# Optimization experiments

Hardware: AMD Instinct MI355X
Metric: run time of the kernel (lower is better)

Reference implementation:

```python
import jax, jax.numpy as jnp
import numpy as np

N_NODES = 50000
N_EDGES = 600000
NFEAT = 256
NHID = 128
NCLASS = 40


def setup_inputs() -> dict:
    key = jax.random.key(0)
    ks = jax.random.split(key, 10)
    x = jax.random.normal(ks[0], (N_NODES, NFEAT), dtype=jnp.float32)
    edge_src = jax.random.randint(ks[1], (N_EDGES,), 0, N_NODES, dtype=jnp.int32)
    edge_dst = jax.random.randint(ks[2], (N_EDGES,), 0, N_NODES, dtype=jnp.int32)
    # normalized adjacency weights (positive, ~1/deg scale)
    edge_weight = jax.random.uniform(ks[3], (N_EDGES,), dtype=jnp.float32) * 0.2
    # GraphConvolution params (Glorot-ish init)
    W1 = jax.random.normal(ks[4], (NFEAT, NHID), dtype=jnp.float32) / np.float32(np.sqrt(NFEAT))
    b1 = jnp.zeros((NHID,), dtype=jnp.float32)
    W2 = jax.random.normal(ks[5], (NHID, NHID), dtype=jnp.float32) / np.float32(np.sqrt(NHID))
    b2 = jnp.zeros((NHID,), dtype=jnp.float32)
    W3 = jax.random.normal(ks[6], (NHID, NCLASS), dtype=jnp.float32) / np.float32(np.sqrt(NHID))
    b3 = jnp.zeros((NCLASS,), dtype=jnp.float32)
    return {"x": x, "edge_weight": edge_weight, "W1": W1, "b1": b1,
            "W2": W2, "b2": b2, "W3": W3, "b3": b3,
            "edge_src": edge_src, "edge_dst": edge_dst}


def _gcn_layer(h, W, b, edge_src, edge_dst, edge_weight):
    # support = h @ W ; out = spmm(adj, support) + b
    support = h @ W                                   # [N, out]
    msgs = support[edge_src] * edge_weight[:, None]   # [E, out]
    agg = jax.ops.segment_sum(msgs, edge_dst, num_segments=N_NODES)
    return agg + b


def reference(x, edge_weight, W1, b1, W2, b2, W3, b3, edge_src, edge_dst):
    # eval mode: F.dropout(training=False) is identity
    h = jax.nn.relu(_gcn_layer(x, W1, b1, edge_src, edge_dst, edge_weight))
    h = jax.nn.relu(_gcn_layer(h, W2, b2, edge_src, edge_dst, edge_weight))
    h = _gcn_layer(h, W3, b3, edge_src, edge_dst, edge_weight)
    return jax.nn.log_softmax(h, axis=1)
```

## Files before the change

kernel.cpp:

```cpp
#include <hip/hip_runtime.h>
#include <math.h>

#define N_NODES 50000
#define N_EDGES 600000
#define NFEAT   256
#define NHID    128
#define NCLASS  40
#define NBUCK 196
#define EPB_A 2048
#define BUCK_CAP 4096
#define BUCK_WIN 5888
#define BINA_BLOCKS ((N_EDGES + EPB_A - 1) / EPB_A)
#define CVTW_BLOCKS 224
#define GEMM_BLOCKS ((N_NODES + 63) / 64)

typedef __attribute__((ext_vector_type(8))) short bf16x8;
typedef __attribute__((ext_vector_type(4))) float f32x4;
typedef __attribute__((ext_vector_type(2))) float f32x2;

__device__ inline ushort f2bf(float f) {
    uint u = __float_as_uint(f);
    uint r = (u + 0x7fffu + ((u >> 16) & 1u)) >> 16;
    return (ushort)r;
}

__global__ __launch_bounds__(256) void binA_cvtw(const int* __restrict__ src,
                                                 const int* __restrict__ dst,
                                                 const float* __restrict__ w,
                                                 int* __restrict__ bucket_cnt,
                                                 int2* __restrict__ staging, int E,
                                                 const float* __restrict__ W1,
                                                 const float* __restrict__ W2,
                                                 const float* __restrict__ W3,
                                                 ushort* __restrict__ BT1,
                                                 ushort* __restrict__ BT2,
                                                 ushort* __restrict__ BT3) {
    int tid = threadIdx.x;
    if ((int)blockIdx.x >= BINA_BLOCKS) {
        int idx = ((int)blockIdx.x - BINA_BLOCKS) * 256 + tid;
        if (idx < 32768) {
            int nr = idx >> 8, k = idx & 255;
            BT1[idx] = f2bf(W1[(size_t)k * 128 + nr]);
        } else if (idx < 49152) {
            int t = idx - 32768;
            int nr = t >> 7, k = t & 127;
            BT2[t] = f2bf(W2[(size_t)k * 128 + nr]);
        } else if (idx < 57344) {
            int t = idx - 49152;
            int nr = t >> 7, k = t & 127;
            BT3[t] = (nr < 40) ? f2bf(W3[(size_t)k * 40 + nr]) : (ushort)0;
        }
        return;
    }
    __shared__ int lh[NBUCK];
    for (int b = tid; b < NBUCK; b += 256) lh[b] = 0;
    __syncthreads();
    int base = blockIdx.x * EPB_A;
    int d[8];
    #pragma unroll
    for (int j = 0; j < 8; ++j) {
        int i = base + j * 256 + tid;
        d[j] = (i < E) ? dst[i] : -1;
        if (d[j] >= 0) atomicAdd(&lh[d[j] >> 8], 1);
    }
    __syncthreads();
    for (int b = tid; b < NBUCK; b += 256) {
        int c = lh[b];
        lh[b] = c ? (b * BUCK_CAP + atomicAdd(&bucket_cnt[b], c)) : 0;
    }
    __syncthreads();
    #pragma unroll
    for (int j = 0; j < 8; ++j) {
        int i = base + j * 256 + tid;
        if (d[j] >= 0) {
            int slot = atomicAdd(&lh[d[j] >> 8], 1);
            uint rec = ((uint)f2bf(w[i]) << 16) | (uint)src[i];
            staging[slot] = make_int2((int)rec, d[j] & 255);
        }
    }
}

template<int NT, bool AF32>
__device__ __forceinline__ void gemm_body(const void* __restrict__ Ain,
                                          const ushort* __restrict__ BT,
                                          int M, int K, int Nout,
                                          ushort* __restrict__ Cout, int row0) {
    __shared__ ushort a_s[64 * 40];
    __shared__ ushort b_s[64 * NT * 40];
    int tid = threadIdx.x;
    int wave = tid >> 6, lane = tid & 63;
    int lr = lane & 15, lk = (lane >> 4) * 8;
    f32x4 acc[4][NT];
    #pragma unroll
    for (int mt = 0; mt < 4; ++mt)
        #pragma unroll
        for (int nt = 0; nt < NT; ++nt) acc[mt][nt] = (f32x4){0.f, 0.f, 0.f, 0.f};

    for (int k0 = 0; k0 < K; k0 += 32) {
        {
            int r = tid >> 2, c8 = (tid & 3) * 8;
            int gr = row0 + r; if (gr >= M) gr = M - 1;
            if (AF32) {
                const float* Af = (const float*)Ain;
                float4 v0 = *(const float4*)(Af + (size_t)gr * K + k0 + c8);
                float4 v1 = *(const float4*)(Af + (size_t)gr * K + k0 + c8 + 4);
                ushort4 o0, o1;
                o0.x = f2bf(v0.x); o0.y = f2bf(v0.y); o0.z = f2bf(v0.z); o0.w = f2bf(v0.w);
                o1.x = f2bf(v1.x); o1.y = f2bf(v1.y); o1.z = f2bf(v1.z); o1.w = f2bf(v1.w);
                *(ushort4*)(a_s + r * 40 + c8) = o0;
                *(ushort4*)(a_s + r * 40 + c8 + 4) = o1;
            } else {
                const ushort* Ab = (const ushort*)Ain;
                float4 v = *(const float4*)(Ab + (size_t)gr * K + k0 + c8);
                *(float4*)(a_s + r * 40 + c8) = v;
            }
        }
        #pragma unroll
        for (int i = 0; i < NT; ++i) {
            int idx = tid * NT + i;
            int r = idx >> 2, c8 = (idx & 3) * 8;
            float4 v = *(const float4*)(BT + (size_t)r * K + k0 + c8);
            *(float4*)(b_s + r * 40 + c8) = v;
        }
        __syncthreads();
        bf16x8 bfr[NT];
        #pragma unroll
        for (int nt = 0; nt < NT; ++nt)
            bfr[nt] = *(const bf16x8*)(b_s + ((wave * NT + nt) * 16 + lr) * 40 + lk);
        #pragma unroll
        for (int mt = 0; mt < 4; ++mt) {
            bf16x8 afr = *(const bf16x8*)(a_s + (mt * 16 + lr) * 40 + lk);
            #pragma unroll
            for (int nt = 0; nt < NT; ++nt)
                acc[mt][nt] = __builtin_amdgcn_mfma_f32_16x16x32_bf16(
                    afr, bfr[nt], acc[mt][nt], 0, 0, 0);
        }
        __syncthreads();
    }
    int col0 = wave * NT * 16;
    #pragma unroll
    for (int mt = 0; mt < 4; ++mt) {
        int gr0 = row0 + mt * 16 + (lane >> 4) * 4;
        #pragma unroll
        for (int nt = 0; nt < NT; ++nt) {
            int gc = col0 + nt * 16 + lr;
            #pragma unroll
            for (int i = 0; i < 4; ++i) {
                int gr = gr0 + i;
                if (gr < M && gc < Nout)
                    Cout[(size_t)gr * Nout + gc] = f2bf(acc[mt][nt][i]);
            }
        }
    }
}

__global__ __launch_bounds__(256) void scan_gemm1(const int* __restrict__ bucket_cnt,
                                                  const int2* __restrict__ staging,
                                                  int2* __restrict__ rsp2,
                                                  uint* __restrict__ edges,
                                                  const float* __restrict__ x,
                                                  const ushort* __restrict__ BT1,
                                                  ushort* __restrict__ supA) {
    if ((int)blockIdx.x >= NBUCK) {
        gemm_body<2, true>(x, BT1, N_NODES, 256, 128, supA,
                           ((int)blockIdx.x - NBUCK) * 64);
        return;
    }
    __shared__ int hist[256];
    __shared__ int buf[256];
    __shared__ int lcur[256];
    int tid = threadIdx.x;
    hist[tid] = 0;
    __syncthreads();
    int b = blockIdx.x;
    int c = bucket_cnt[b];
    const int2* st = staging + (size_t)b * BUCK_CAP;
    for (int p = tid; p < c; p += 256) atomicAdd(&hist[st[p].y], 1);
    __syncthreads();
    int v = (hist[tid] + 7) & ~7;
    buf[tid] = v;
    __syncthreads();
    #pragma unroll
    for (int off = 1; off < 256; off <<= 1) {
        int t = (tid >= off) ? buf[tid - off] : 0;
        __syncthreads();
        buf[tid] += t;
        __syncthreads();
    }
    int bb = b * BUCK_WIN;
    int ex = buf[tid] - v + bb;
    int i = b * 256 + tid;
    if (i < N_NODES) rsp2[i] = make_int2(ex, ex + v);
    lcur[tid] = ex;
    __syncthreads();
    int e0 = bb + buf[255];
    for (int p = bb + tid; p < e0; p += 256) edges[p] = 0;
    __syncthreads();
    for (int p = tid; p < c; p += 256) {
        int2 r = st[p];
        int slot = atomicAdd(&lcur[r.y], 1);
        edges[slot] = (uint)r.x;
    }
}

template<int NT>
__global__ __launch_bounds__(256) void fused_spmm_gemm(const uint* __restrict__ sup,
                                                       const int2* __restrict__ rsp2,
                                                       const uint* __restrict__ edges,
                                                       const float* __restrict__ bias,
                                                       const ushort* __restrict__ BT,
                                                       int Nout,
                                                       ushort* __restrict__ Cout) {
    __shared__ ushort a4_s[4][64 * 40];
    int tid = threadIdx.x;
    int wave = tid >> 6, lane = tid & 63;
    int row0 = blockIdx.x * 64;
    float bx = bias[2 * lane], by = bias[2 * lane + 1];
    int ks = lane >> 4;
    int kk = 2 * (lane & 15);
    for (int i = 0; i < 16; ++i) {
        int node = row0 + wave * 16 + i;
        int nd = (node < N_NODES) ? node : (N_NODES - 1);
        int2 ke = rsp2[nd];
        int k = ke.x, e = ke.y;
        f32x2 acc2 = (f32x2){0.f, 0.f};
        if (k < e) {
            const uint4* q4 = (const uint4*)(edges + k);
            uint4 qa = q4[0], qb = q4[1];
            for (; k < e; k += 8) {
                int kn = k + 8;
                int kc = (kn < e) ? kn : k;
                const uint4* n4 = (const uint4*)(edges + kc);
                uint4 na = n4[0], nb = n4[1];
                uint q[8] = {qa.x, qa.y, qa.z, qa.w, qb.x, qb.y, qb.z, qb.w};
                uint p[8];
                #pragma unroll
                for (int j = 0; j < 8; ++j)
                    p[j] = sup[(size_t)(q[j] & 0xffffu) * 64 + lane];
                #pragma unroll
                for (int j = 0; j < 8; ++j) {
                    float w = __uint_as_float(q[j] & 0xffff0000u);
                    f32x2 v;
                    v.x = __uint_as_float(p[j] << 16);
                    v.y = __uint_as_float(p[j] & 0xffff0000u);
                    acc2 += v * (f32x2){w, w};
                }
                qa = na; qb = nb;
            }
        }
        uint pk = ((uint)f2bf(fmaxf(acc2.y + by, 0.f)) << 16)
                |  (uint)f2bf(fmaxf(acc2.x + bx, 0.f));
        *(uint*)(&a4_s[ks][(wave * 16 + i) * 40 + kk]) = pk;
    }
    __syncthreads();
    int lr = lane & 15, lk = (lane >> 4) * 8;
    f32x4 acc[4][NT];
    #pragma unroll
    for (int mt = 0; mt < 4; ++mt)
        #pragma unroll
        for (int nt = 0; nt < NT; ++nt) acc[mt][nt] = (f32x4){0.f, 0.f, 0.f, 0.f};
    #pragma unroll
    for (int ksi = 0; ksi < 4; ++ksi) {
        int k0 = ksi * 32;
        bf16x8 bfr[NT];
        #pragma unroll
        for (int nt = 0; nt < NT; ++nt)
            bfr[nt] = *(const bf16x8*)(BT +
                (size_t)((wave * NT + nt) * 16 + lr) * 128 + k0 + lk);
        #pragma unroll
        for (int mt = 0; mt < 4; ++mt) {
            bf16x8 afr = *(const bf16x8*)(&a4_s[ksi][(mt * 16 + lr) * 40 + lk]);
            #pragma unroll
            for (int nt = 0; nt < NT; ++nt)
                acc[mt][nt] = __builtin_amdgcn_mfma_f32_16x16x32_bf16(
                    afr, bfr[nt], acc[mt][nt], 0, 0, 0);
        }
    }
    int col0 = wave * NT * 16;
    #pragma unroll
    for (int mt = 0; mt < 4; ++mt) {
        int gr0 = row0 + mt * 16 + (lane >> 4) * 4;
        #pragma unroll
        for (int nt = 0; nt < NT; ++nt) {
            int gc = col0 + nt * 16 + lr;
            #pragma unroll
            for (int i = 0; i < 4; ++i) {
                int gr = gr0 + i;
                if (gr < N_NODES && gc < Nout)
                    Cout[(size_t)gr * Nout + gc] = f2bf(acc[mt][nt][i]);
            }
        }
    }
}

__global__ __launch_bounds__(256) void spmm40_lsm(const ushort* __restrict__ sup,
                                                  const int2* __restrict__ rsp2,
                                                  const uint* __restrict__ edges,
                                                  const float* __restrict__ bias,
                                                  float* __restrict__ out, int n) {
    int wid = blockIdx.x * 4 + (threadIdx.x >> 6);
    int lane = threadIdx.x & 63;
    if (wid >= n) return;
    int2 ke = rsp2[wid];
    int k = ke.x, e = ke.y;
    float acc = 0.f;
    int lf = (lane < 40) ? lane : 39;
    if (k < e) {
        const uint4* q4 = (const uint4*)(edges + k);
        uint4 qa = q4[0], qb = q4[1];
        for (; k < e; k += 8) {
            int kn = k + 8;
            int kc = (kn < e) ? kn : k;
            const uint4* n4 = (const uint4*)(edges + kc);
            uint4 na = n4[0], nb4 = n4[1];
            uint q[8] = {qa.x, qa.y, qa.z, qa.w, qb.x, qb.y, qb.z, qb.w};
            float p[8];
            #pragma unroll
            for (int j = 0; j < 8; ++j) {
                uint us = sup[(size_t)(q[j] & 0xffffu) * 40 + lf];
                p[j] = __uint_as_float(us << 16);
            }
            #pragma unroll
            for (int j = 0; j < 8; ++j)
                acc += p[j] * __uint_as_float(q[j] & 0xffff0000u);
            qa = na; qb = nb4;
        }
    }
    float v = (lane < 40) ? acc + bias[lane] : -INFINITY;
    float m = v;
    #pragma unroll
    for (int off = 32; off; off >>= 1) m = fmaxf(m, __shfl_xor(m, off, 64));
    float ex = (lane < 40) ? expf(v - m) : 0.f;
    float s = ex;
    #pragma unroll
    for (int off = 32; off; off >>= 1) s += __shfl_xor(s, off, 64);
    float ls = logf(s);
    if (lane < 40) out[(size_t)wid * 40 + lane] = v - m - ls;
}

extern "C" void kernel_launch(void* const* d_in, const int* in_sizes, int n_in,
                              void* d_out, int out_size, void* d_ws, size_t ws_size,
                              hipStream_t stream) {
    const float* x   = (const float*)d_in[0];
    const float* ew  = (const float*)d_in[1];
    const float* W1  = (const float*)d_in[2];
    const float* b1  = (const float*)d_in[3];
    const float* W2  = (const float*)d_in[4];
    const float* b2  = (const float*)d_in[5];
    const float* W3  = (const float*)d_in[6];
    const float* b3  = (const float*)d_in[7];
    const int* esrc  = (const int*)d_in[8];
    const int* edst  = (const int*)d_in[9];
    float* out = (float*)d_out;

    char* ws = (char*)d_ws;
    size_t off = 0;
    auto alloc = [&](size_t bytes) {
        size_t cur = off;
        off += (bytes + 255) & ~(size_t)255;
        return cur;
    };
    int* bucket_cnt = (int*)(ws + alloc(256 * sizeof(int)));
    int2* rsp2   = (int2*)(ws + alloc((size_t)N_NODES * sizeof(int2)));
    uint* edges  = (uint*)(ws + alloc((size_t)NBUCK * BUCK_WIN * sizeof(uint)));
    int2* staging = (int2*)(ws + alloc((size_t)NBUCK * BUCK_CAP * sizeof(int2)));
    ushort* BT1  = (ushort*)(ws + alloc(128 * 256 * 2));
    ushort* BT2  = (ushort*)(ws + alloc(128 * 128 * 2));
    ushort* BT3  = (ushort*)(ws + alloc(64 * 128 * 2));
    char* Sreg   = ws + alloc((size_t)N_NODES * 128 * 2);
    char* Hreg   = ws + alloc((size_t)N_NODES * 128 * 2);

    ushort* supA = (ushort*)Sreg;
    ushort* supB = (ushort*)Hreg;
    ushort* sup3 = (ushort*)Sreg;

    hipMemsetAsync(bucket_cnt, 0, 256 * sizeof(int), stream);
    binA_cvtw<<<BINA_BLOCKS + CVTW_BLOCKS, 256, 0, stream>>>(
        esrc, edst, ew, bucket_cnt, staging, N_EDGES, W1, W2, W3, BT1, BT2, BT3);
    scan_gemm1<<<NBUCK + GEMM_BLOCKS, 256, 0, stream>>>(
        bucket_cnt, staging, rsp2, edges, x, BT1, supA);
    fused_spmm_gemm<2><<<GEMM_BLOCKS, 256, 0, stream>>>(
        (const uint*)supA, rsp2, edges, b1, BT2, 128, supB);
    fused_spmm_gemm<1><<<GEMM_BLOCKS, 256, 0, stream>>>(
        (const uint*)supB, rsp2, edges, b2, BT3, 40, sup3);
    spmm40_lsm<<<(N_NODES + 3) / 4, 256, 0, stream>>>(sup3, rsp2, edges, b3,
                                                      out, N_NODES);
}
```

Measured before the change: 231.2 us.

## Stream each wave's 16-row edge range as one software-pipelined gather loop

The aggregation phase now treats the 16 destination rows of a wave as one contiguous edge range. It loads 16-edge records double-buffered, prefetching the next record and gathering one chunk while accumulating the previous, and flushes each row's result at its segment boundary. This removes the per-row loop startup and pipeline drain, keeping more gathers in flight across short rows. In exchange it needs more registers (two 16-entry buffers), adds a clamp on the gather index for reads past the range, and over-allocates workspace so prefetches beyond the end stay in bounds.

```diff
diff --git a/kernel.cpp b/kernel.cpp
--- a/kernel.cpp
+++ b/kernel.cpp
@@ -203,56 +203,102 @@
     }
 }
 
+
+#define LDREC(Ra, Rb, Rc, Rd, POS) do { \
+    const uint4* _p = (const uint4*)(edges + (POS)); \
+    Ra = _p[0]; Rb = _p[1]; Rc = _p[2]; Rd = _p[3]; \
+} while (0)
+
+#define GATHER(P, W, Ra, Rb, Rc, Rd) do { \
+    uint _r[16] = {Ra.x, Ra.y, Ra.z, Ra.w, Rb.x, Rb.y, Rb.z, Rb.w, \
+                   Rc.x, Rc.y, Rc.z, Rc.w, Rd.x, Rd.y, Rd.z, Rd.w}; \
+    _Pragma("unroll") \
+    for (int _j = 0; _j < 16; ++_j) { \
+        uint _idx = _r[_j] & 0xffffu; \
+        if (_idx >= N_NODES) _idx = N_NODES - 1;   \
+        P[_j] = sup[(size_t)_idx * 64 + lane]; \
+        W[_j] = __uint_as_float(_r[_j] & 0xffff0000u); \
+    } \
+} while (0)
+
+#define FLUSH1() do { \
+    uint _pk = ((uint)f2bf(fmaxf(acc2.y + by, 0.f)) << 16) \
+             |  (uint)f2bf(fmaxf(acc2.x + bx, 0.f)); \
+    *(uint*)(&a4_s[ks][(wave * 16 + cur) * 40 + kk]) = _pk; \
+    acc2 = (f32x2){0.f, 0.f}; \
+    ++cur; \
+    e_cur = (cur < 16) ? e_s[wave][cur + 1] : 0x7fffffff; \
+} while (0)
+
+#define FMA_CHUNK(QB, P, W) do { \
+    _Pragma("unroll") \
+    for (int _g = 0; _g < 2; ++_g) { \
+        int _qg = (QB) + _g * 8; \
+        while (cur < 16 && _qg >= e_cur) FLUSH1(); \
+        if (_qg < QE) { \
+            _Pragma("unroll") \
+            for (int _j = 0; _j < 8; ++_j) { \
+                uint _pv = P[_g * 8 + _j]; \
+                f32x2 _v; \
+                _v.x = __uint_as_float(_pv << 16); \
+                _v.y = __uint_as_float(_pv & 0xffff0000u); \
+                float _w = W[_g * 8 + _j]; \
+                acc2 += _v * (f32x2){_w, _w}; \
+            } \
+        } \
+    } \
+} while (0)
+
 template<int NT>
-__global__ __launch_bounds__(256) void fused_spmm_gemm(const uint* __restrict__ sup,
-                                                       const int2* __restrict__ rsp2,
-                                                       const uint* __restrict__ edges,
-                                                       const float* __restrict__ bias,
-                                                       const ushort* __restrict__ BT,
-                                                       int Nout,
-                                                       ushort* __restrict__ Cout) {
+__device__ __forceinline__ void fused_body(const uint* __restrict__ sup,
+                                           const int2* __restrict__ rsp2,
+                                           const uint* __restrict__ edges,
+                                           const float* __restrict__ bias,
+                                           const ushort* __restrict__ BT,
+                                           int Nout,
+                                           ushort* __restrict__ Cout) {
     __shared__ ushort a4_s[4][64 * 40];
+    __shared__ int e_s[4][17];
     int tid = threadIdx.x;
     int wave = tid >> 6, lane = tid & 63;
     int row0 = blockIdx.x * 64;
+    int nfirst = row0 + wave * 16;
     float bx = bias[2 * lane], by = bias[2 * lane + 1];
     int ks = lane >> 4;
     int kk = 2 * (lane & 15);
-    for (int i = 0; i < 16; ++i) {
-        int node = row0 + wave * 16 + i;
-        int nd = (node < N_NODES) ? node : (N_NODES - 1);
-        int2 ke = rsp2[nd];
-        int k = ke.x, e = ke.y;
-        f32x2 acc2 = (f32x2){0.f, 0.f};
-        if (k < e) {
-            const uint4* q4 = (const uint4*)(edges + k);
-            uint4 qa = q4[0], qb = q4[1];
-            for (; k < e; k += 8) {
-                int kn = k + 8;
-                int kc = (kn < e) ? kn : k;
-                const uint4* n4 = (const uint4*)(edges + kc);
-                uint4 na = n4[0], nb = n4[1];
-                uint q[8] = {qa.x, qa.y, qa.z, qa.w, qb.x, qb.y, qb.z, qb.w};
-                uint p[8];
-                #pragma unroll
-                for (int j = 0; j < 8; ++j)
-                    p[j] = sup[(size_t)(q[j] & 0xffffu) * 64 + lane];
-                #pragma unroll
-                for (int j = 0; j < 8; ++j) {
-                    float w = __uint_as_float(q[j] & 0xffff0000u);
-                    f32x2 v;
-                    v.x = __uint_as_float(p[j] << 16);
-                    v.y = __uint_as_float(p[j] & 0xffff0000u);
-                    acc2 += v * (f32x2){w, w};
-                }
-                qa = na; qb = nb;
-            }
-        }
-        uint pk = ((uint)f2bf(fmaxf(acc2.y + by, 0.f)) << 16)
-                |  (uint)f2bf(fmaxf(acc2.x + bx, 0.f));
-        *(uint*)(&a4_s[ks][(wave * 16 + i) * 40 + kk]) = pk;
-    }
-    __syncthreads();
+
+    if (lane < 16) {
+        int nd = nfirst + lane; if (nd >= N_NODES) nd = N_NODES - 1;
+        int2 t = rsp2[nd];
+        e_s[wave][lane + 1] = t.y;
+        if (lane == 0) e_s[wave][0] = t.x;
+    }
+    __syncthreads();
+    int Q = e_s[wave][0], QE = e_s[wave][16];
+    int cur = 0, e_cur = e_s[wave][1];
+    f32x2 acc2 = (f32x2){0.f, 0.f};
+
+    uint4 rA0, rA1, rA2, rA3, rB0, rB1, rB2, rB3;
+    uint pa[16], pb[16];
+    float wa[16], wb[16];
+    int q = Q;
+    LDREC(rA0, rA1, rA2, rA3, q);
+    GATHER(pa, wa, rA0, rA1, rA2, rA3);
+    LDREC(rB0, rB1, rB2, rB3, q + 16);
+    while (q < QE) {
+        GATHER(pb, wb, rB0, rB1, rB2, rB3);
+        LDREC(rA0, rA1, rA2, rA3, q + 32);
+        FMA_CHUNK(q, pa, wa);
+        q += 16;
+        if (q >= QE) break;
+        GATHER(pa, wa, rA0, rA1, rA2, rA3);
+        LDREC(rB0, rB1, rB2, rB3, q + 32);
+        FMA_CHUNK(q, pb, wb);
+        q += 16;
+    }
+    while (cur < 16) FLUSH1();
+    __syncthreads();
+
     int lr = lane & 15, lk = (lane >> 4) * 8;
     f32x4 acc[4][NT];
     #pragma unroll
@@ -291,6 +337,24 @@
             }
         }
     }
+}
+
+__global__ __launch_bounds__(256) void fused_ag2(const uint* __restrict__ sup,
+                                                 const int2* __restrict__ rsp2,
+                                                 const uint* __restrict__ edges,
+                                                 const float* __restrict__ bias,
+                                                 const ushort* __restrict__ BT,
+                                                 ushort* __restrict__ Cout) {
+    fused_body<2>(sup, rsp2, edges, bias, BT, 128, Cout);
+}
+
+__global__ __launch_bounds__(256) void fused_ag3(const uint* __restrict__ sup,
+                                                 const int2* __restrict__ rsp2,
+                                                 const uint* __restrict__ edges,
+                                                 const float* __restrict__ bias,
+                                                 const ushort* __restrict__ BT,
+                                                 ushort* __restrict__ Cout) {
+    fused_body<1>(sup, rsp2, edges, bias, BT, 40, Cout);
 }
 
 __global__ __launch_bounds__(256) void spmm40_lsm(const ushort* __restrict__ sup,
@@ -369,6 +433,7 @@
     ushort* BT3  = (ushort*)(ws + alloc(64 * 128 * 2));
     char* Sreg   = ws + alloc((size_t)N_NODES * 128 * 2);
     char* Hreg   = ws + alloc((size_t)N_NODES * 128 * 2);
+    (void)alloc((size_t)66000 * 128 * 2);
 
     ushort* supA = (ushort*)Sreg;
     ushort* supB = (ushort*)Hreg;
@@ -379,10 +444,10 @@
         esrc, edst, ew, bucket_cnt, staging, N_EDGES, W1, W2, W3, BT1, BT2, BT3);
     scan_gemm1<<<NBUCK + GEMM_BLOCKS, 256, 0, stream>>>(
         bucket_cnt, staging, rsp2, edges, x, BT1, supA);
-    fused_spmm_gemm<2><<<GEMM_BLOCKS, 256, 0, stream>>>(
-        (const uint*)supA, rsp2, edges, b1, BT2, 128, supB);
-    fused_spmm_gemm<1><<<GEMM_BLOCKS, 256, 0, stream>>>(
-        (const uint*)supB, rsp2, edges, b2, BT3, 40, sup3);
+    fused_ag2<<<GEMM_BLOCKS, 256, 0, stream>>>(
+        (const uint*)supA, rsp2, edges, b1, BT2, supB);
+    fused_ag3<<<GEMM_BLOCKS, 256, 0, stream>>>(
+        (const uint*)supB, rsp2, edges, b2, BT3, sup3);
     spmm40_lsm<<<(N_NODES + 3) / 4, 256, 0, stream>>>(sup3, rsp2, edges, b3,
                                                       out, N_NODES);
 }
```

Result: faster. 216.2 us (-6.5%).
